# Kernel tuning notes

Measured on AMD Instinct MI355X. Metric: run time of the kernel, lower is better.

## Reference

```python
import jax, jax.numpy as jnp
import numpy as np

B, H, KVH, D = 16, 32, 8, 128
MAX_CTX = 4096
NUM_SLOTS = 131072


def setup_inputs() -> dict:
    key = jax.random.key(0)
    k1, k2, k3, k4, k5 = jax.random.split(key, 5)
    query = jax.random.normal(k1, (B, H, D), dtype=jnp.float32)
    key_cache = jax.random.normal(k2, (NUM_SLOTS, KVH, D), dtype=jnp.float32)
    value_cache = jax.random.normal(k3, (NUM_SLOTS, KVH, D), dtype=jnp.float32)
    slot_indices = jax.random.randint(k4, (B, MAX_CTX), 0, NUM_SLOTS, dtype=jnp.int32)
    # at least 1 valid token per sequence (module zeros fully-empty seqs; avoid NaN softmax)
    context_lens = jax.random.randint(k5, (B,), 1, MAX_CTX + 1, dtype=jnp.int32)
    return {
        "query": query,
        "key_cache": key_cache,
        "value_cache": value_cache,
        "slot_indices": slot_indices,
        "context_lens": context_lens,
    }


def reference(query, key_cache, value_cache, slot_indices, context_lens):
    b, h, d = query.shape
    kvh = key_cache.shape[1]
    g = h // kvh  # GQA group size (repeat_interleave on kv heads)
    scale = 1.0 / d ** 0.5

    # paged gather: per-token slot lookup from flat KV pool -> [B, S, KVH, D]
    K = key_cache[slot_indices]
    V = value_cache[slot_indices]

    # heads grouped as [kv_head, group] matches repeat_interleave(dim=0)
    q = query.reshape(b, kvh, g, d)
    scores = jnp.einsum('bkgd,bskd->bkgs', q, K) * scale  # [B, KVH, G, S]

    s = slot_indices.shape[1]
    valid = jnp.arange(s)[None, :] < context_lens[:, None]  # [B, S]
    scores = jnp.where(valid[:, None, None, :], scores, -jnp.inf)
    attn = jax.nn.softmax(scores, axis=-1)

    out = jnp.einsum('bkgs,bskd->bkgd', attn, V)  # [B, KVH, G, D]
    return out.reshape(b, h, d)
```

## Files before the change

### kernel.cpp

```cpp
#include <hip/hip_runtime.h>
#include <hip/hip_bf16.h>


namespace {
constexpr int B_ = 16;
constexpr int H_ = 32;
constexpr int KVH_ = 8;
constexpr int D_ = 128;
constexpr int G_ = H_ / KVH_;
constexpr int MAX_CTX_ = 4096;
constexpr int PART_ = 128;
constexpr int NPART_ = MAX_CTX_ / PART_;
constexpr float SCALE_ = 0.088388347648318447f;
constexpr int PSTRIDE_ = G_ * D_ + 2 * G_;
}

__global__ __launch_bounds__(256) void pa_partial(
    const float* __restrict__ q,
    const float* __restrict__ kc,
    const float* __restrict__ vc,
    const int* __restrict__ slots,
    const int* __restrict__ ctx_lens,
    float* __restrict__ ws)
{
  const int part = blockIdx.x;
  const int kvh  = blockIdx.y;
  const int b    = blockIdx.z;
  const int ctx  = ctx_lens[b];
  const int t0   = part * PART_;
  if (t0 >= ctx) return;
  const int t1 = min(t0 + PART_, ctx);

  const int tid  = threadIdx.x;
  const int wid  = tid >> 6;
  const int lane = tid & 63;
  const int grp  = lane >> 4;
  const int sub  = lane & 15;

  float4 qa[G_], qb[G_];
#pragma unroll
  for (int g = 0; g < G_; ++g) {
    const float* qp = q + ((size_t)b * H_ + (size_t)(kvh * G_ + g)) * D_ + 8 * sub;
    qa[g] = *(const float4*)qp;
    qb[g] = *(const float4*)(qp + 4);
    qa[g].x *= SCALE_; qa[g].y *= SCALE_; qa[g].z *= SCALE_; qa[g].w *= SCALE_;
    qb[g].x *= SCALE_; qb[g].y *= SCALE_; qb[g].z *= SCALE_; qb[g].w *= SCALE_;
  }

  float m[G_], l[G_];
  float4 aa[G_], ab[G_];
#pragma unroll
  for (int g = 0; g < G_; ++g) {
    m[g] = -INFINITY;
    l[g] = 0.f;
    aa[g] = make_float4(0.f, 0.f, 0.f, 0.f);
    ab[g] = make_float4(0.f, 0.f, 0.f, 0.f);
  }

  const int* sp = slots + (size_t)b * MAX_CTX_;
  const int tmax = t1 - 1;
  const int lead = wid * 4 + grp;

  int t_cur = t0 + lead;
  int slot_cur = sp[min(t_cur, tmax)];
  int slot_nxt = sp[min(t_cur + 16, tmax)];

  const int doff = 8 * sub;
  size_t roff = ((size_t)slot_cur * KVH_ + kvh) * D_ + doff;
  float4 k0 = *(const float4*)(kc + roff);
  float4 k1 = *(const float4*)(kc + roff + 4);
  float4 v0 = *(const float4*)(vc + roff);
  float4 v1 = *(const float4*)(vc + roff + 4);

  for (int base = t0; base < t1; base += 16) {
    const int slot_n2 = sp[min(base + 32 + lead, tmax)];
    const size_t noff = ((size_t)slot_nxt * KVH_ + kvh) * D_ + doff;
    const float4 nk0 = *(const float4*)(kc + noff);
    const float4 nk1 = *(const float4*)(kc + noff + 4);
    const float4 nv0 = *(const float4*)(vc + noff);
    const float4 nv1 = *(const float4*)(vc + noff + 4);

    const int t = base + lead;
    if (t < t1) {
      float s[G_];
#pragma unroll
      for (int g = 0; g < G_; ++g) {
        s[g] = qa[g].x * k0.x + qa[g].y * k0.y + qa[g].z * k0.z + qa[g].w * k0.w
             + qb[g].x * k1.x + qb[g].y * k1.y + qb[g].z * k1.z + qb[g].w * k1.w;
      }
#pragma unroll
      for (int g = 0; g < G_; ++g) {
#pragma unroll
        for (int o = 1; o < 16; o <<= 1) s[g] += __shfl_xor(s[g], o, 64);
      }
      const bool need = (s[0] > m[0] + 8.f) | (s[1] > m[1] + 8.f) |
                        (s[2] > m[2] + 8.f) | (s[3] > m[3] + 8.f);
      if (need) {
#pragma unroll
        for (int g = 0; g < G_; ++g) {
          const float mn = fmaxf(m[g], s[g]);
          const float c = __expf(m[g] - mn);
          m[g] = mn; l[g] *= c;
          aa[g].x *= c; aa[g].y *= c; aa[g].z *= c; aa[g].w *= c;
          ab[g].x *= c; ab[g].y *= c; ab[g].z *= c; ab[g].w *= c;
        }
      }
#pragma unroll
      for (int g = 0; g < G_; ++g) {
        const float p = __expf(s[g] - m[g]);
        l[g] += p;
        aa[g].x += p * v0.x; aa[g].y += p * v0.y;
        aa[g].z += p * v0.z; aa[g].w += p * v0.w;
        ab[g].x += p * v1.x; ab[g].y += p * v1.y;
        ab[g].z += p * v1.z; ab[g].w += p * v1.w;
      }
    }
    k0 = nk0; k1 = nk1; v0 = nv0; v1 = nv1;
    slot_nxt = slot_n2;
  }

#pragma unroll
  for (int o = 16; o <= 32; o <<= 1) {
#pragma unroll
    for (int g = 0; g < G_; ++g) {
      const float mo = __shfl_xor(m[g], o, 64);
      const float lo = __shfl_xor(l[g], o, 64);
      float4 ao, bo;
      ao.x = __shfl_xor(aa[g].x, o, 64); ao.y = __shfl_xor(aa[g].y, o, 64);
      ao.z = __shfl_xor(aa[g].z, o, 64); ao.w = __shfl_xor(aa[g].w, o, 64);
      bo.x = __shfl_xor(ab[g].x, o, 64); bo.y = __shfl_xor(ab[g].y, o, 64);
      bo.z = __shfl_xor(ab[g].z, o, 64); bo.w = __shfl_xor(ab[g].w, o, 64);
      const float M = fmaxf(m[g], mo);
      const bool dead = (M == -INFINITY);
      const float c1 = dead ? 0.f : __expf(m[g] - M);
      const float c2 = dead ? 0.f : __expf(mo - M);
      l[g] = l[g] * c1 + lo * c2;
      aa[g].x = aa[g].x * c1 + ao.x * c2; aa[g].y = aa[g].y * c1 + ao.y * c2;
      aa[g].z = aa[g].z * c1 + ao.z * c2; aa[g].w = aa[g].w * c1 + ao.w * c2;
      ab[g].x = ab[g].x * c1 + bo.x * c2; ab[g].y = ab[g].y * c1 + bo.y * c2;
      ab[g].z = ab[g].z * c1 + bo.z * c2; ab[g].w = ab[g].w * c1 + bo.w * c2;
      m[g] = M;
    }
  }

  __shared__ float sm_[4][G_];
  __shared__ float sl_[4][G_];
  __shared__ float sa_[4][G_][16][8];
  if (grp == 0) {
#pragma unroll
    for (int g = 0; g < G_; ++g) {
      *(float4*)&sa_[wid][g][sub][0] = aa[g];
      *(float4*)&sa_[wid][g][sub][4] = ab[g];
    }
    if (sub == 0) {
#pragma unroll
      for (int g = 0; g < G_; ++g) { sm_[wid][g] = m[g]; sl_[wid][g] = l[g]; }
    }
  }
  __syncthreads();

  const int g = wid;
  const float M = fmaxf(fmaxf(sm_[0][g], sm_[1][g]),
                        fmaxf(sm_[2][g], sm_[3][g]));
  const int si = lane >> 2;
  const int sj = (2 * lane) & 7;
  float L = 0.f, Ox = 0.f, Oy = 0.f;
#pragma unroll
  for (int w = 0; w < 4; ++w) {
    const float c = __expf(sm_[w][g] - M);
    L += sl_[w][g] * c;
    Ox += sa_[w][g][si][sj] * c;
    Oy += sa_[w][g][si][sj + 1] * c;
  }
  float* wp = ws + (((size_t)b * KVH_ + kvh) * NPART_ + part) * PSTRIDE_;
  *(float2*)(wp + g * D_ + 2 * lane) = make_float2(Ox, Oy);
  if (lane == 0) {
    wp[G_ * D_ + g] = M;
    wp[G_ * D_ + G_ + g] = L;
  }
}

__global__ __launch_bounds__(512) void pa_reduce(
    const float* __restrict__ ws,
    const int* __restrict__ ctx_lens,
    float* __restrict__ out)
{
  const int bk = blockIdx.x;
  const int b = bk / KVH_;
  const int kvh = bk % KVH_;
  const int g = threadIdx.x >> 7;
  const int d = threadIdx.x & 127;
  const int ctx = ctx_lens[b];
  int np = (ctx + PART_ - 1) / PART_;
  if (np > NPART_) np = NPART_;

  const float* base = ws + ((size_t)b * KVH_ + kvh) * NPART_ * PSTRIDE_;

  float M = -INFINITY;
  for (int p = 0; p < np; ++p)
    M = fmaxf(M, base[p * PSTRIDE_ + G_ * D_ + g]);

  float L = 0.f, O = 0.f;
  for (int p = 0; p < np; ++p) {
    const float mp = base[p * PSTRIDE_ + G_ * D_ + g];
    const float lp = base[p * PSTRIDE_ + G_ * D_ + G_ + g];
    const float c = __expf(mp - M);
    L += lp * c;
    O += base[p * PSTRIDE_ + g * D_ + d] * c;
  }
  out[((size_t)b * H_ + (size_t)(kvh * G_ + g)) * D_ + d] = O / L;
}

extern "C" void kernel_launch(void* const* d_in, const int* in_sizes, int n_in,
                              void* d_out, int out_size, void* d_ws, size_t ws_size,
                              hipStream_t stream) {
  const float* q     = (const float*)d_in[0];
  const float* kc    = (const float*)d_in[1];
  const float* vc    = (const float*)d_in[2];
  const int*   slots = (const int*)d_in[3];
  const int*   lens  = (const int*)d_in[4];
  float* out = (float*)d_out;
  float* ws  = (float*)d_ws;

  dim3 grid1(NPART_, KVH_, B_);
  pa_partial<<<grid1, 256, 0, stream>>>(q, kc, vc, slots, lens, ws);
  pa_reduce<<<B_ * KVH_, 512, 0, stream>>>(ws, lens, out);
}
```

Measured before the change: 73.66 us.

## Map KV heads to waves within a block and halve partition length

The partial kernel now launches one 512-thread block per (partition, batch), and each wave handles one KV head. Before, one 256-thread block ran per (partition, KV head, batch) and its four waves split the tokens. Partitions shrink from 128 to 64 tokens, which removes the shared-memory cross-wave merge and the __syncthreads. The eight waves of a block now read all KV heads of the same slots, so each slot's contiguous K/V row is gathered by one block. In exchange, each wave runs a longer serial token loop, the reduce kernel merges twice as many partitions, and the final store indexes the register arrays by runtime group, which may force scratch memory.

Result: slower. 105.0 us (+42.5%).

```diff
diff --git a/kernel.cpp b/kernel.cpp
--- a/kernel.cpp
+++ b/kernel.cpp
@@ -9,13 +9,13 @@
 constexpr int D_ = 128;
 constexpr int G_ = H_ / KVH_;
 constexpr int MAX_CTX_ = 4096;
-constexpr int PART_ = 128;
+constexpr int PART_ = 64;
 constexpr int NPART_ = MAX_CTX_ / PART_;
 constexpr float SCALE_ = 0.088388347648318447f;
 constexpr int PSTRIDE_ = G_ * D_ + 2 * G_;
 }
 
-__global__ __launch_bounds__(256) void pa_partial(
+__global__ __launch_bounds__(512) void pa_partial(
     const float* __restrict__ q,
     const float* __restrict__ kc,
     const float* __restrict__ vc,
@@ -24,15 +24,14 @@
     float* __restrict__ ws)
 {
   const int part = blockIdx.x;
-  const int kvh  = blockIdx.y;
-  const int b    = blockIdx.z;
+  const int b    = blockIdx.y;
   const int ctx  = ctx_lens[b];
   const int t0   = part * PART_;
   if (t0 >= ctx) return;
   const int t1 = min(t0 + PART_, ctx);
 
   const int tid  = threadIdx.x;
-  const int wid  = tid >> 6;
+  const int kvh  = tid >> 6;
   const int lane = tid & 63;
   const int grp  = lane >> 4;
   const int sub  = lane & 15;
@@ -59,11 +58,9 @@
 
   const int* sp = slots + (size_t)b * MAX_CTX_;
   const int tmax = t1 - 1;
-  const int lead = wid * 4 + grp;
-
-  int t_cur = t0 + lead;
-  int slot_cur = sp[min(t_cur, tmax)];
-  int slot_nxt = sp[min(t_cur + 16, tmax)];
+
+  int slot_cur = sp[min(t0 + grp,     tmax)];
+  int slot_nxt = sp[min(t0 + 4 + grp, tmax)];
 
   const int doff = 8 * sub;
   size_t roff = ((size_t)slot_cur * KVH_ + kvh) * D_ + doff;
@@ -72,15 +69,15 @@
   float4 v0 = *(const float4*)(vc + roff);
   float4 v1 = *(const float4*)(vc + roff + 4);
 
-  for (int base = t0; base < t1; base += 16) {
-    const int slot_n2 = sp[min(base + 32 + lead, tmax)];
+  for (int base = t0; base < t1; base += 4) {
+    const int slot_n2 = sp[min(base + 8 + grp, tmax)];
     const size_t noff = ((size_t)slot_nxt * KVH_ + kvh) * D_ + doff;
     const float4 nk0 = *(const float4*)(kc + noff);
     const float4 nk1 = *(const float4*)(kc + noff + 4);
     const float4 nv0 = *(const float4*)(vc + noff);
     const float4 nv1 = *(const float4*)(vc + noff + 4);
 
-    const int t = base + lead;
+    const int t = base + grp;
     if (t < t1) {
       float s[G_];
 #pragma unroll
@@ -143,40 +140,15 @@
     }
   }
 
-  __shared__ float sm_[4][G_];
-  __shared__ float sl_[4][G_];
-  __shared__ float sa_[4][G_][16][8];
-  if (grp == 0) {
+  float* wp = ws + (((size_t)b * KVH_ + kvh) * NPART_ + part) * PSTRIDE_;
+  *(float4*)(wp + grp * D_ + doff)     = aa[grp];
+  *(float4*)(wp + grp * D_ + doff + 4) = ab[grp];
+  if (lane == 0) {
 #pragma unroll
     for (int g = 0; g < G_; ++g) {
-      *(float4*)&sa_[wid][g][sub][0] = aa[g];
-      *(float4*)&sa_[wid][g][sub][4] = ab[g];
+      wp[G_ * D_ + g]      = m[g];
+      wp[G_ * D_ + G_ + g] = l[g];
     }
-    if (sub == 0) {
-#pragma unroll
-      for (int g = 0; g < G_; ++g) { sm_[wid][g] = m[g]; sl_[wid][g] = l[g]; }
-    }
-  }
-  __syncthreads();
-
-  const int g = wid;
-  const float M = fmaxf(fmaxf(sm_[0][g], sm_[1][g]),
-                        fmaxf(sm_[2][g], sm_[3][g]));
-  const int si = lane >> 2;
-  const int sj = (2 * lane) & 7;
-  float L = 0.f, Ox = 0.f, Oy = 0.f;
-#pragma unroll
-  for (int w = 0; w < 4; ++w) {
-    const float c = __expf(sm_[w][g] - M);
-    L += sl_[w][g] * c;
-    Ox += sa_[w][g][si][sj] * c;
-    Oy += sa_[w][g][si][sj + 1] * c;
-  }
-  float* wp = ws + (((size_t)b * KVH_ + kvh) * NPART_ + part) * PSTRIDE_;
-  *(float2*)(wp + g * D_ + 2 * lane) = make_float2(Ox, Oy);
-  if (lane == 0) {
-    wp[G_ * D_ + g] = M;
-    wp[G_ * D_ + G_ + g] = L;
   }
 }
 
@@ -222,7 +194,7 @@
   float* out = (float*)d_out;
   float* ws  = (float*)d_ws;
 
-  dim3 grid1(NPART_, KVH_, B_);
-  pa_partial<<<grid1, 256, 0, stream>>>(q, kc, vc, slots, lens, ws);
+  dim3 grid1(NPART_, B_);
+  pa_partial<<<grid1, 512, 0, stream>>>(q, kc, vc, slots, lens, ws);
   pa_reduce<<<B_ * KVH_, 512, 0, stream>>>(ws, lens, out);
 }
```
